# Optimization experiments

Measured on AMD Instinct MI355X. Metric: run time of the kernel, lower is better.

## Reference

```python
import jax, jax.numpy as jnp
import numpy as np


def _shift_lr(t):
    # t: [B, L, H] -> (left, right) neighbor states with zero padding
    B, L, H = t.shape
    pad = jnp.zeros((B, 1, H), dtype=t.dtype)
    left = jnp.concatenate([pad, t[:, :-1, :]], axis=1)
    right = jnp.concatenate([t[:, 1:, :], pad], axis=1)
    return left, right


def setup_inputs() -> dict:
    key = jax.random.key(0)
    ks = jax.random.split(key, 7)
    B, L, H = 32, 2048, 256
    h_t = jax.random.normal(ks[0], (B, L, H), dtype=jnp.float32)
    x = jax.random.normal(ks[1], (B, L, H), dtype=jnp.float32)
    h_slot = jax.random.normal(ks[2], (B, L, H), dtype=jnp.float32)
    h_intent = jax.random.normal(ks[3], (B, L, H), dtype=jnp.float32)
    c_t = jax.random.normal(ks[4], (B, L, H), dtype=jnp.float32)
    # gate order: [i, o, f, l, r, u]; linear in = 6H, out = H
    Ws = jax.random.normal(ks[5], (6, 6 * H, H), dtype=jnp.float32) * 0.02
    bs = jnp.zeros((6, H), dtype=jnp.float32)
    return {"h_t": h_t, "x": x, "h_slot": h_slot, "h_intent": h_intent,
            "c_t": c_t, "Ws": Ws, "bs": bs}


def reference(h_t, x, h_slot, h_intent, c_t, Ws, bs):
    h_left, h_right = _shift_lr(h_t)
    # concat order: [h_mid, h_left, h_right, x, h_slot, h_intent] -> [B,L,6H]
    cat = jnp.concatenate([h_t, h_left, h_right, x, h_slot, h_intent], axis=-1)
    # one batched GEMM for all six gates: [6, B, L, H]
    gates = jnp.einsum('blc,gch->gblh', cat, Ws) + bs[:, None, None, :]
    i_t = jax.nn.sigmoid(gates[0])
    o_t = jax.nn.sigmoid(gates[1])
    f_t = jax.nn.sigmoid(gates[2])
    l_t = jax.nn.sigmoid(gates[3])
    r_t = jax.nn.sigmoid(gates[4])
    u_t = jnp.tanh(gates[5])
    # softmax across the 4 gates (axis 0 of the stack)
    soft = jax.nn.softmax(jnp.stack([i_t, f_t, l_t, r_t], axis=0), axis=0)
    i_t, f_t, l_t, r_t = soft[0], soft[1], soft[2], soft[3]
    c_left, c_right = _shift_lr(c_t)
    c_new = f_t * c_t + l_t * c_left + r_t * c_right + i_t * u_t
    h_new = o_t * jnp.tanh(c_new)
    return (h_new, c_new)
```

## Files before the change

kernel.cpp:

```cpp
#include <hip/hip_runtime.h>

typedef __attribute__((ext_vector_type(8))) short short8;
typedef __attribute__((ext_vector_type(4))) float f32x4;

#define BB 32
#define LL 2048
#define HH 256
#define MTOT (BB*LL)
#define KK 1536
#define HSIZE (MTOT*HH)

#define SWZ4(v) (((v) & 3) ^ (((v) >> 2) & 3))

__device__ __forceinline__ unsigned short f2bf(float f){
    unsigned u = __builtin_bit_cast(unsigned, f);
    u += 0x7FFFu + ((u >> 16) & 1u);
    return (unsigned short)(u >> 16);
}
__device__ __forceinline__ unsigned pk2(float lo, float hi){
    return (unsigned)f2bf(lo) | ((unsigned)f2bf(hi) << 16);
}
__device__ __forceinline__ float sigm(float v){
    return 1.0f / (1.0f + __expf(-v));
}
__device__ __forceinline__ float ftanh(float v){
    v = fminf(fmaxf(v, -30.0f), 30.0f);
    float e = __expf(2.0f * v);
    return (e - 1.0f) / (e + 1.0f);
}
__device__ __forceinline__ void gload_lds16(const void* g, void* l){
    __builtin_amdgcn_global_load_lds(
        (const __attribute__((address_space(1))) unsigned int*)g,
        (__attribute__((address_space(3))) unsigned int*)l, 16, 0, 0);
}

__global__ __launch_bounds__(256) void prep_bt(const float* __restrict__ Ws,
                                               unsigned short* __restrict__ Bt){
    __shared__ float tile[64][65];
    int bid = blockIdx.x;
    int kb = bid % 24; int tmp = bid / 24; int hb = tmp & 3; int g = tmp >> 2;
    int t = threadIdx.x;
    const float* src = Ws + (size_t)g * (KK * HH) + (size_t)(kb * 64) * HH + hb * 64;
    #pragma unroll
    for (int it = 0; it < 16; ++it){
        int e = it * 256 + t; int kk = e >> 6, hh = e & 63;
        tile[kk][hh] = src[(size_t)kk * HH + hh];
    }
    __syncthreads();
    #pragma unroll
    for (int it = 0; it < 2; ++it){
        int jj  = t;
        int ksl = it;
        int hc  = jj >> 2, qp = jj & 3;
        int col = g * 64 + hc;
        int q   = qp ^ SWZ4(col);
        int kbase = ksl * 32 + q * 8;
        unsigned wz[4];
        #pragma unroll
        for (int p = 0; p < 4; ++p)
            wz[p] = pk2(tile[kbase + 2*p][hc], tile[kbase + 2*p + 1][hc]);
        int ksg = kb * 2 + ksl;
        size_t off = ((size_t)(hb * 48 + ksg) * 1536 + (size_t)g * 256 + jj) * 8;
        *(uint4*)&Bt[off] = *(uint4*)wz;
    }
}

__global__ __launch_bounds__(256) void prep_a16(
    const float* __restrict__ h_t, const float* __restrict__ x,
    const float* __restrict__ h_slot, const float* __restrict__ h_intent,
    unsigned short* __restrict__ A16)
{
    const size_t nslots = (size_t)4 * HSIZE / 8;
    for (size_t s = (size_t)blockIdx.x * 256 + threadIdx.x; s < nslots;
         s += (size_t)gridDim.x * 256){
        size_t tsr = s >> 21;
        size_t w   = s & ((1u << 21) - 1);
        const float* src = (tsr == 0) ? h_t : (tsr == 1) ? x
                         : (tsr == 2) ? h_slot : h_intent;
        const float4 v0 = *(const float4*)(src + w * 8);
        const float4 v1 = *(const float4*)(src + w * 8 + 4);
        uint4 o;
        o.x = pk2(v0.x, v0.y); o.y = pk2(v0.z, v0.w);
        o.z = pk2(v1.x, v1.y); o.w = pk2(v1.z, v1.w);
        *(uint4*)(A16 + s * 8) = o;
    }
}

__global__ __launch_bounds__(512, 2) void slstm_fused2(
    const unsigned short* __restrict__ A16, const float* __restrict__ c_t,
    const float* __restrict__ bs, const unsigned short* __restrict__ Bt,
    float* __restrict__ out)
{
    __shared__ __align__(16) unsigned short As[2][128 * 32];
    __shared__ __align__(16) unsigned short Bs[2][384 * 32];

    const int t    = threadIdx.x;
    const int wv   = t >> 6,  ln  = t & 63;
    const int rg   = wv >> 2, ht  = wv & 3;
    const int quad = ln >> 4, l16 = ln & 15;

    const int rawb = blockIdx.x;
    const int vb   = (rawb & 7) * 256 + (rawb >> 3);
    const int h_chunk = vb & 3;
    const int m_block = vb >> 2;
    const int h0      = h_chunk * 64;

    const int  arow = t >> 2;
    const int  aq   = t & 3;
    const int  asq  = (aq ^ SWZ4(arow)) << 3;
    const long mg   = (long)m_block * 128 + arow;
    const int  qa   = (quad ^ SWZ4(l16)) << 3;

    const unsigned short* BtH = Bt + (size_t)h_chunk * 48 * 1536 * 8;

    f32x4 acc[4][6] = {};

    auto stageA = [&](int buf, int ks){
        int c = ks >> 3; int tsel, sh;
        switch (c){
            case 0:  tsel = 0; sh =  0; break;
            case 1:  tsel = 0; sh = -1; break;
            case 2:  tsel = 0; sh =  1; break;
            case 3:  tsel = 1; sh =  0; break;
            case 4:  tsel = 2; sh =  0; break;
            default: tsel = 3; sh =  0; break;
        }
        long srow = mg + sh;
        srow = srow < 0 ? 0 : (srow > (long)MTOT - 1 ? (long)MTOT - 1 : srow);
        const unsigned short* src =
            A16 + (size_t)tsel * HSIZE + (size_t)srow * HH + ((ks & 7) << 5) + asq;
        gload_lds16(src, &As[buf][wv * 16 * 32]);
    };
    auto stageB = [&](int buf, int ks){
        const unsigned short* gsrc = BtH + (size_t)ks * 1536 * 8;
        #pragma unroll
        for (int i = 0; i < 3; ++i){
            gload_lds16(gsrc + (size_t)(i * 512 + t) * 8,
                        &Bs[buf][(i * 512 + wv * 64) * 8]);
        }
    };

    stageA(0, 0);
    stageB(0, 0);
    __syncthreads();

    const bool mb_first = (m_block & 15) == 0;
    const bool mb_last  = (m_block & 15) == 15;

    for (int ks = 0; ks < 48; ++ks){
        const int cur = ks & 1, nxt = cur ^ 1;

        {
            int c = ks >> 3;
            bool fix0   = (c == 1) && mb_first;
            bool fix127 = (c == 2) && mb_last;
            if (fix0 || fix127){
                int br = fix0 ? 0 : 127;
                if (t < 4) *(uint4*)&As[cur][br * 32 + t * 8] = make_uint4(0,0,0,0);
                __syncthreads();
            }
        }

        if (ks < 47){
            stageA(nxt, ks + 1);
            stageB(nxt, ks + 1);
        }

        short8 a[4];
        #pragma unroll
        for (int mt = 0; mt < 4; ++mt)
            a[mt] = *(const short8*)&As[cur][(rg * 64 + mt * 16 + l16) * 32 + qa];
        #pragma unroll
        for (int g = 0; g < 6; ++g){
            short8 bfrag = *(const short8*)&Bs[cur][(g * 64 + ht * 16 + l16) * 32 + qa];
            #pragma unroll
            for (int mt = 0; mt < 4; ++mt)
                acc[mt][g] = __builtin_amdgcn_mfma_f32_16x16x32_bf16(a[mt], bfrag, acc[mt][g], 0, 0, 0);
        }
        __syncthreads();
    }

    const int h = h0 + ht * 16 + l16;
    float bias[6];
    #pragma unroll
    for (int g = 0; g < 6; ++g) bias[g] = bs[g * HH + h];

    #pragma unroll
    for (int mt = 0; mt < 4; ++mt){
        #pragma unroll
        for (int r = 0; r < 4; ++r){
            long row = (long)m_block * 128 + rg * 64 + mt * 16 + quad * 4 + r;
            int  ls  = (int)(row & (LL - 1));
            float gi = sigm(acc[mt][0][r] + bias[0]);
            float go = sigm(acc[mt][1][r] + bias[1]);
            float gf = sigm(acc[mt][2][r] + bias[2]);
            float gl = sigm(acc[mt][3][r] + bias[3]);
            float gr = sigm(acc[mt][4][r] + bias[4]);
            float gu = ftanh(acc[mt][5][r] + bias[5]);
            float ei = __expf(gi), ef = __expf(gf), el = __expf(gl), er = __expf(gr);
            float inv = 1.0f / (ei + ef + el + er);
            float cm  = c_t[row * HH + h];
            float clv = (ls > 0)      ? c_t[(row - 1) * HH + h] : 0.0f;
            float crv = (ls < LL - 1) ? c_t[(row + 1) * HH + h] : 0.0f;
            float cn  = (ef * cm + el * clv + er * crv + ei * gu) * inv;
            float hn  = go * ftanh(cn);
            out[row * HH + h]         = hn;
            out[HSIZE + row * HH + h] = cn;
        }
    }
}

__global__ __launch_bounds__(512, 2) void slstm_fused(
    const float* __restrict__ h_t, const float* __restrict__ x,
    const float* __restrict__ h_slot, const float* __restrict__ h_intent,
    const float* __restrict__ c_t, const float* __restrict__ bs,
    const unsigned short* __restrict__ Bt, float* __restrict__ out)
{
    __shared__ __align__(16) unsigned short As[2][128 * 32];
    __shared__ __align__(16) unsigned short Bs[2][384 * 32];

    const int t    = threadIdx.x;
    const int wv   = t >> 6,  ln  = t & 63;
    const int rg   = wv >> 2, ht  = wv & 3;
    const int quad = ln >> 4, l16 = ln & 15;

    const int rawb = blockIdx.x;
    const int vb   = (rawb & 7) * 256 + (rawb >> 3);
    const int h_chunk = vb & 3;
    const int m_block = vb >> 2;
    const int h0      = h_chunk * 64;

    const int  arow = t >> 2;
    const int  aq   = t & 3;
    const int  akq  = aq << 3;
    const long mg   = (long)m_block * 128 + arow;
    const int  lseq = (int)(mg & (LL - 1));
    const int  awq  = (aq ^ SWZ4(arow)) << 3;
    const int  qa   = (quad ^ SWZ4(l16)) << 3;

    const unsigned short* BtH = Bt + (size_t)h_chunk * 48 * 1536 * 8;

    f32x4 acc[4][6] = {};

    float4 av0, av1;
    auto stageA_issue = [&](int ks){
        int c  = ks >> 3;
        int kk = ((ks & 7) << 5) + akq;
        const float* src; int sh;
        switch (c){
            case 0:  src = h_t;      sh =  0; break;
            case 1:  src = h_t;      sh = -1; break;
            case 2:  src = h_t;      sh =  1; break;
            case 3:  src = x;        sh =  0; break;
            case 4:  src = h_slot;   sh =  0; break;
            default: src = h_intent; sh =  0; break;
        }
        int sl = lseq + sh;
        av0 = make_float4(0.f,0.f,0.f,0.f); av1 = av0;
        if ((unsigned)sl < (unsigned)LL){
            const float* p = src + ((mg + sh) * HH + kk);
            av0 = *(const float4*)p;
            av1 = *(const float4*)(p + 4);
        }
    };
    auto stageB = [&](int buf, int ks){
        const unsigned short* gsrc = BtH + (size_t)ks * 1536 * 8;
        #pragma unroll
        for (int i = 0; i < 3; ++i){
            gload_lds16(gsrc + (size_t)(i * 512 + t) * 8,
                        &Bs[buf][(i * 512 + wv * 64) * 8]);
        }
    };
    auto stageA_write = [&](int buf){
        uint4 w;
        w.x = pk2(av0.x, av0.y); w.y = pk2(av0.z, av0.w);
        w.z = pk2(av1.x, av1.y); w.w = pk2(av1.z, av1.w);
        *(uint4*)&As[buf][arow * 32 + awq] = w;
    };

    stageA_issue(0);
    stageB(0, 0);
    stageA_write(0);
    __syncthreads();

    for (int ks = 0; ks < 48; ++ks){
        const int cur = ks & 1, nxt = cur ^ 1;
        if (ks < 47){
            stageA_issue(ks + 1);
            stageB(nxt, ks + 1);
        }
        short8 a[4];
        #pragma unroll
        for (int mt = 0; mt < 4; ++mt)
            a[mt] = *(const short8*)&As[cur][(rg * 64 + mt * 16 + l16) * 32 + qa];
        #pragma unroll
        for (int g = 0; g < 6; ++g){
            short8 bfrag = *(const short8*)&Bs[cur][(g * 64 + ht * 16 + l16) * 32 + qa];
            #pragma unroll
            for (int mt = 0; mt < 4; ++mt)
                acc[mt][g] = __builtin_amdgcn_mfma_f32_16x16x32_bf16(a[mt], bfrag, acc[mt][g], 0, 0, 0);
        }
        if (ks < 47) stageA_write(nxt);
        __syncthreads();
    }

    const int h = h0 + ht * 16 + l16;
    float bias[6];
    #pragma unroll
    for (int g = 0; g < 6; ++g) bias[g] = bs[g * HH + h];

    #pragma unroll
    for (int mt = 0; mt < 4; ++mt){
        #pragma unroll
        for (int r = 0; r < 4; ++r){
            long row = (long)m_block * 128 + rg * 64 + mt * 16 + quad * 4 + r;
            int  ls  = (int)(row & (LL - 1));
            float gi = sigm(acc[mt][0][r] + bias[0]);
            float go = sigm(acc[mt][1][r] + bias[1]);
            float gf = sigm(acc[mt][2][r] + bias[2]);
            float gl = sigm(acc[mt][3][r] + bias[3]);
            float gr = sigm(acc[mt][4][r] + bias[4]);
            float gu = ftanh(acc[mt][5][r] + bias[5]);
            float ei = __expf(gi), ef = __expf(gf), el = __expf(gl), er = __expf(gr);
            float inv = 1.0f / (ei + ef + el + er);
            float cm  = c_t[row * HH + h];
            float clv = (ls > 0)      ? c_t[(row - 1) * HH + h] : 0.0f;
            float crv = (ls < LL - 1) ? c_t[(row + 1) * HH + h] : 0.0f;
            float cn  = (ef * cm + el * clv + er * crv + ei * gu) * inv;
            float hn  = go * ftanh(cn);
            out[row * HH + h]         = hn;
            out[HSIZE + row * HH + h] = cn;
        }
    }
}

extern "C" void kernel_launch(void* const* d_in, const int* in_sizes, int n_in,
                              void* d_out, int out_size, void* d_ws, size_t ws_size,
                              hipStream_t stream){
    const float* h_t      = (const float*)d_in[0];
    const float* x        = (const float*)d_in[1];
    const float* h_slot   = (const float*)d_in[2];
    const float* h_intent = (const float*)d_in[3];
    const float* c_t      = (const float*)d_in[4];
    const float* Ws       = (const float*)d_in[5];
    const float* bs       = (const float*)d_in[6];

    unsigned short* Bt = (unsigned short*)d_ws;
    const size_t bt_elems = (size_t)KK * KK;
    const size_t need = bt_elems * 2 + (size_t)4 * HSIZE * 2;

    prep_bt<<<576, 256, 0, stream>>>(Ws, Bt);

    if (ws_size >= need){
        unsigned short* A16 = Bt + bt_elems;
        prep_a16<<<4096, 256, 0, stream>>>(h_t, x, h_slot, h_intent, A16);
        slstm_fused2<<<2048, 512, 0, stream>>>(A16, c_t, bs, Bt, (float*)d_out);
    } else {
        slstm_fused<<<2048, 512, 0, stream>>>(h_t, x, h_slot, h_intent, c_t, bs, Bt, (float*)d_out);
    }
}
```

Before: 866.2 us.

## Merge prep kernels and overlap next-tile loads with compute via explicit waitcnt

Combines the weight-transpose and activation-to-bf16 prep kernels into one launch, removing one kernel launch and its serialization. In the main GEMM loop, the next k-step's global-to-LDS loads are now issued before the barrier, and a partial vmcnt wait allows them to overlap with the current step's MFMAs. The full __syncthreads are replaced by raw s_barrier calls, the edge-row zeroing is limited to the owning wave, s_setprio is raised around the MFMA block, and the bias load is hoisted before the loop. This relies on the vmcnt(4) count matching the outstanding loads (1 A plus 3 B per step), so a count error could cause LDS races.

```diff
diff --git a/kernel.cpp b/kernel.cpp
--- a/kernel.cpp
+++ b/kernel.cpp
@@ -34,10 +34,9 @@
         (__attribute__((address_space(3))) unsigned int*)l, 16, 0, 0);
 }
 
-__global__ __launch_bounds__(256) void prep_bt(const float* __restrict__ Ws,
-                                               unsigned short* __restrict__ Bt){
+__device__ __forceinline__ void prep_bt_body(int bid, const float* __restrict__ Ws,
+                                             unsigned short* __restrict__ Bt){
     __shared__ float tile[64][65];
-    int bid = blockIdx.x;
     int kb = bid % 24; int tmp = bid / 24; int hb = tmp & 3; int g = tmp >> 2;
     int t = threadIdx.x;
     const float* src = Ws + (size_t)g * (KK * HH) + (size_t)(kb * 64) * HH + hb * 64;
@@ -65,14 +64,14 @@
     }
 }
 
-__global__ __launch_bounds__(256) void prep_a16(
+__device__ __forceinline__ void prep_a16_body(int bid, int nblk,
     const float* __restrict__ h_t, const float* __restrict__ x,
     const float* __restrict__ h_slot, const float* __restrict__ h_intent,
     unsigned short* __restrict__ A16)
 {
     const size_t nslots = (size_t)4 * HSIZE / 8;
-    for (size_t s = (size_t)blockIdx.x * 256 + threadIdx.x; s < nslots;
-         s += (size_t)gridDim.x * 256){
+    for (size_t s = (size_t)bid * 256 + threadIdx.x; s < nslots;
+         s += (size_t)nblk * 256){
         size_t tsr = s >> 21;
         size_t w   = s & ((1u << 21) - 1);
         const float* src = (tsr == 0) ? h_t : (tsr == 1) ? x
@@ -86,6 +85,21 @@
     }
 }
 
+__global__ __launch_bounds__(256) void prep_all(
+    const float* __restrict__ Ws,
+    const float* __restrict__ h_t, const float* __restrict__ x,
+    const float* __restrict__ h_slot, const float* __restrict__ h_intent,
+    unsigned short* __restrict__ Bt, unsigned short* __restrict__ A16)
+{
+    if (blockIdx.x < 4096) prep_a16_body(blockIdx.x, 4096, h_t, x, h_slot, h_intent, A16);
+    else                   prep_bt_body(blockIdx.x - 4096, Ws, Bt);
+}
+
+__global__ __launch_bounds__(256) void prep_bt(const float* __restrict__ Ws,
+                                               unsigned short* __restrict__ Bt){
+    prep_bt_body(blockIdx.x, Ws, Bt);
+}
+
 __global__ __launch_bounds__(512, 2) void slstm_fused2(
     const unsigned short* __restrict__ A16, const float* __restrict__ c_t,
     const float* __restrict__ bs, const unsigned short* __restrict__ Bt,
@@ -112,6 +126,11 @@
     const int  qa   = (quad ^ SWZ4(l16)) << 3;
 
     const unsigned short* BtH = Bt + (size_t)h_chunk * 48 * 1536 * 8;
+
+    const int h = h0 + ht * 16 + l16;
+    float bias[6];
+    #pragma unroll
+    for (int g = 0; g < 6; ++g) bias[g] = bs[g * HH + h];
 
     f32x4 acc[4][6] = {};
 
@@ -142,13 +161,22 @@
 
     stageA(0, 0);
     stageB(0, 0);
-    __syncthreads();
+    asm volatile("s_waitcnt vmcnt(0)" ::: "memory");
+    __builtin_amdgcn_s_barrier();
 
     const bool mb_first = (m_block & 15) == 0;
     const bool mb_last  = (m_block & 15) == 15;
 
     for (int ks = 0; ks < 48; ++ks){
         const int cur = ks & 1, nxt = cur ^ 1;
+
+        if (ks < 47){
+            stageA(nxt, ks + 1);
+            stageB(nxt, ks + 1);
+            asm volatile("s_waitcnt vmcnt(4)" ::: "memory");
+        } else {
+            asm volatile("s_waitcnt vmcnt(0)" ::: "memory");
+        }
 
         {
             int c = ks >> 3;
@@ -156,20 +184,20 @@
             bool fix127 = (c == 2) && mb_last;
             if (fix0 || fix127){
                 int br = fix0 ? 0 : 127;
-                if (t < 4) *(uint4*)&As[cur][br * 32 + t * 8] = make_uint4(0,0,0,0);
-                __syncthreads();
+                int ow = br >> 4;
+                if (wv == ow && ln < 4)
+                    *(uint4*)&As[cur][br * 32 + ln * 8] = make_uint4(0,0,0,0);
+                asm volatile("s_waitcnt lgkmcnt(0)" ::: "memory");
             }
         }
 
-        if (ks < 47){
-            stageA(nxt, ks + 1);
-            stageB(nxt, ks + 1);
-        }
+        __builtin_amdgcn_s_barrier();
 
         short8 a[4];
         #pragma unroll
         for (int mt = 0; mt < 4; ++mt)
             a[mt] = *(const short8*)&As[cur][(rg * 64 + mt * 16 + l16) * 32 + qa];
+        __builtin_amdgcn_s_setprio(1);
         #pragma unroll
         for (int g = 0; g < 6; ++g){
             short8 bfrag = *(const short8*)&Bs[cur][(g * 64 + ht * 16 + l16) * 32 + qa];
@@ -177,13 +205,11 @@
             for (int mt = 0; mt < 4; ++mt)
                 acc[mt][g] = __builtin_amdgcn_mfma_f32_16x16x32_bf16(a[mt], bfrag, acc[mt][g], 0, 0, 0);
         }
-        __syncthreads();
-    }
-
-    const int h = h0 + ht * 16 + l16;
-    float bias[6];
-    #pragma unroll
-    for (int g = 0; g < 6; ++g) bias[g] = bs[g * HH + h];
+        __builtin_amdgcn_s_setprio(0);
+
+        asm volatile("s_waitcnt lgkmcnt(0)" ::: "memory");
+        __builtin_amdgcn_s_barrier();
+    }
 
     #pragma unroll
     for (int mt = 0; mt < 4; ++mt){
@@ -349,13 +375,12 @@
     const size_t bt_elems = (size_t)KK * KK;
     const size_t need = bt_elems * 2 + (size_t)4 * HSIZE * 2;
 
-    prep_bt<<<576, 256, 0, stream>>>(Ws, Bt);
-
     if (ws_size >= need){
         unsigned short* A16 = Bt + bt_elems;
-        prep_a16<<<4096, 256, 0, stream>>>(h_t, x, h_slot, h_intent, A16);
+        prep_all<<<4672, 256, 0, stream>>>(Ws, h_t, x, h_slot, h_intent, Bt, A16);
         slstm_fused2<<<2048, 512, 0, stream>>>(A16, c_t, bs, Bt, (float*)d_out);
     } else {
+        prep_bt<<<576, 256, 0, stream>>>(Ws, Bt);
         slstm_fused<<<2048, 512, 0, stream>>>(h_t, x, h_slot, h_intent, c_t, bs, Bt, (float*)d_out);
     }
 }
```

Result: slower. 890.2 us (+2.8%).
